# Kernel tuning notes

Measured on AMD Instinct MI355X. Metric: run time of the kernel, lower is better.

The kernel has to match this reference:

```python
import jax, jax.numpy as jnp
import numpy as np

N = 100000
E = 1600000
D = 128
L = 4
G = 64
EPS = 1e-5


def _bn(x, g, b, m, v):
    # BatchNorm1d in eval mode: normalize with running stats
    return (x - m) * jax.lax.rsqrt(v + EPS) * g + b


def setup_inputs() -> dict:
    key = jax.random.key(0)
    ks = jax.random.split(key, 32)
    x = jax.random.normal(ks[0], (N, 11), jnp.float32)
    pos = jax.random.normal(ks[1], (N, 3), jnp.float32)
    edge_index = jax.random.randint(ks[2], (2, E), 0, N)
    edge_attr = jax.random.normal(ks[3], (E, 4), jnp.float32)
    batch = jnp.sort(jax.random.randint(ks[4], (N,), 0, G))
    s = 0.05
    lin_in_w = jax.random.normal(ks[5], (14, D), jnp.float32) * s
    lin_in_b = jnp.zeros((D,), jnp.float32)
    msg_w1 = jax.random.normal(ks[6], (L, 2 * D + 4, D), jnp.float32) * s
    msg_b1 = jnp.zeros((L, D), jnp.float32)
    msg_bn_g = jnp.ones((L, D), jnp.float32)
    msg_bn_b = jnp.zeros((L, D), jnp.float32)
    msg_bn_m = jax.random.normal(ks[7], (L, D), jnp.float32) * s
    msg_bn_v = jax.random.uniform(ks[8], (L, D), jnp.float32, 0.5, 1.5)
    msg_w2 = jax.random.normal(ks[9], (L, D, D), jnp.float32) * s
    msg_b2 = jnp.zeros((L, D), jnp.float32)
    upd_w1 = jax.random.normal(ks[10], (L, 2 * D, D), jnp.float32) * s
    upd_b1 = jnp.zeros((L, D), jnp.float32)
    upd_bn_g = jnp.ones((L, D), jnp.float32)
    upd_bn_b = jnp.zeros((L, D), jnp.float32)
    upd_bn_m = jax.random.normal(ks[11], (L, D), jnp.float32) * s
    upd_bn_v = jax.random.uniform(ks[12], (L, D), jnp.float32, 0.5, 1.5)
    upd_w2 = jax.random.normal(ks[13], (L, D, D), jnp.float32) * s
    upd_b2 = jnp.zeros((L, D), jnp.float32)
    pred_w = jax.random.normal(ks[14], (D, 1), jnp.float32) * s
    pred_b = jnp.zeros((1,), jnp.float32)
    return dict(x=x, pos=pos, edge_index=edge_index, edge_attr=edge_attr, batch=batch,
                lin_in_w=lin_in_w, lin_in_b=lin_in_b,
                msg_w1=msg_w1, msg_b1=msg_b1, msg_bn_g=msg_bn_g, msg_bn_b=msg_bn_b,
                msg_bn_m=msg_bn_m, msg_bn_v=msg_bn_v, msg_w2=msg_w2, msg_b2=msg_b2,
                upd_w1=upd_w1, upd_b1=upd_b1, upd_bn_g=upd_bn_g, upd_bn_b=upd_bn_b,
                upd_bn_m=upd_bn_m, upd_bn_v=upd_bn_v, upd_w2=upd_w2, upd_b2=upd_b2,
                pred_w=pred_w, pred_b=pred_b)


def reference(x, pos, edge_index, edge_attr, batch,
              lin_in_w, lin_in_b,
              msg_w1, msg_b1, msg_bn_g, msg_bn_b, msg_bn_m, msg_bn_v, msg_w2, msg_b2,
              upd_w1, upd_b1, upd_bn_g, upd_bn_b, upd_bn_m, upd_bn_v, upd_w2, upd_b2,
              pred_w, pred_b):
    src = edge_index[0]  # j (source)
    dst = edge_index[1]  # i (target, aggregation index)
    h = jnp.concatenate([x, pos], axis=-1) @ lin_in_w + lin_in_b  # [N, D]
    for l in range(L):
        # message: cat(h_i, h_j, edge_attr) -> Linear -> ReLU -> BN -> Linear -> ReLU
        m = jnp.concatenate([h[dst], h[src], edge_attr], axis=-1)  # [E, 2D+4]
        m = jax.nn.relu(m @ msg_w1[l] + msg_b1[l])
        m = _bn(m, msg_bn_g[l], msg_bn_b[l], msg_bn_m[l], msg_bn_v[l])
        m = jax.nn.relu(m @ msg_w2[l] + msg_b2[l])  # [E, D]
        # aggregate: scatter-add on target nodes
        aggr = jax.ops.segment_sum(m, dst, num_segments=N)  # [N, D]
        # update: cat(h, aggr) -> Linear -> ReLU -> BN -> Linear -> ReLU
        u = jnp.concatenate([h, aggr], axis=-1)
        u = jax.nn.relu(u @ upd_w1[l] + upd_b1[l])
        u = _bn(u, upd_bn_g[l], upd_bn_b[l], upd_bn_m[l], upd_bn_v[l])
        u = jax.nn.relu(u @ upd_w2[l] + upd_b2[l])
        h = h + u  # residual
    # global mean pool over graphs
    sums = jax.ops.segment_sum(h, batch, num_segments=G)
    cnts = jax.ops.segment_sum(jnp.ones((N,), h.dtype), batch, num_segments=G)
    h_graph = sums / jnp.maximum(cnts, 1.0)[:, None]
    out = h_graph @ pred_w + pred_b  # [G, 1]
    return out.reshape(-1)
```

## Files before the change

### kernel.cpp

```cpp
#include <hip/hip_runtime.h>
#include <hip/hip_bf16.h>


#define EPSBN 1e-5f
#define TS 136
#define AS 264

typedef __bf16 bf16x8 __attribute__((ext_vector_type(8)));
typedef float floatx4 __attribute__((ext_vector_type(4)));

static __device__ __forceinline__ unsigned short f2b(float f) {
  union { float f; unsigned u; } v; v.f = f;
  unsigned u = v.u;
  return (unsigned short)((u + 0x7fffu + ((u >> 16) & 1u)) >> 16);
}
static __device__ __forceinline__ unsigned pk2(float lo, float hi) {
  union { __hip_bfloat162 h; unsigned u; } v;
  v.h = __float22bfloat162_rn(make_float2(lo, hi));
  return v.u;
}
static __device__ __forceinline__ float ubits(unsigned u) {
  union { unsigned u; float f; } v; v.u = u; return v.f;
}

__global__ __launch_bounds__(128) void fold_kernel(
    const float* __restrict__ mw2, const float* __restrict__ mb2,
    const float* __restrict__ mg, const float* __restrict__ mb,
    const float* __restrict__ mm, const float* __restrict__ mv,
    const float* __restrict__ uw2, const float* __restrict__ ub2,
    const float* __restrict__ ug, const float* __restrict__ ub,
    const float* __restrict__ um, const float* __restrict__ uv,
    unsigned short* __restrict__ mW2fT, float* __restrict__ mB2f,
    unsigned short* __restrict__ uW2fT, float* __restrict__ uB2f) {
  int l = blockIdx.x & 3;
  bool isu = blockIdx.x >= 4;
  const float* W2 = (isu ? uw2 : mw2) + (size_t)l * 128 * 128;
  const float* b2 = (isu ? ub2 : mb2) + l * 128;
  const float* gg = (isu ? ug : mg) + l * 128;
  const float* bb = (isu ? ub : mb) + l * 128;
  const float* mn = (isu ? um : mm) + l * 128;
  const float* vr = (isu ? uv : mv) + l * 128;
  unsigned short* WfT = (isu ? uW2fT : mW2fT) + (size_t)l * 128 * 128;
  float* Bf = (isu ? uB2f : mB2f) + l * 128;
  __shared__ float a[128], c[128];
  int d = threadIdx.x;
  float ad = gg[d] * rsqrtf(vr[d] + EPSBN);
  a[d] = ad;
  c[d] = bb[d] - mn[d] * ad;
  __syncthreads();
  float acc = b2[d];
  for (int k = 0; k < 128; ++k) {
    float w = W2[k * 128 + d];
    WfT[(size_t)d * 128 + k] = f2b(a[k] * w);
    acc = fmaf(c[k], w, acc);
  }
  Bf[d] = acc;
}

__global__ __launch_bounds__(256) void transp_kernel(
    const float* __restrict__ mw1, const float* __restrict__ uw1,
    unsigned short* __restrict__ W1abT, unsigned short* __restrict__ U1T) {
  int l = blockIdx.x & 3;
  bool isu = blockIdx.x >= 4;
  int tid = threadIdx.x;
  if (!isu) {
    const float* W = mw1 + (size_t)l * 260 * 128;
    unsigned short* T = W1abT + (size_t)l * 256 * 128;
    for (int i = tid; i < 256 * 128; i += 256) {
      int n = i >> 7, k = i & 127;
      float v = (n < 128) ? W[(size_t)k * 128 + n] : W[(size_t)(128 + k) * 128 + (n - 128)];
      T[i] = f2b(v);
    }
  } else {
    const float* W = uw1 + (size_t)l * 256 * 128;
    unsigned short* T = U1T + (size_t)l * 128 * 256;
    for (int i = tid; i < 128 * 256; i += 256) {
      int n = i >> 8, k = i & 255;
      T[i] = f2b(W[(size_t)k * 128 + n]);
    }
  }
}

__global__ __launch_bounds__(256) void lin_in_kernel(
    const float* __restrict__ x, const float* __restrict__ pos,
    const float* __restrict__ W, const float* __restrict__ b,
    float* __restrict__ h, int Nn) {
  int gi = blockIdx.x * 256 + threadIdx.x;
  if (gi >= Nn * 128) return;
  int n = gi >> 7, d = gi & 127;
  float acc = b[d];
#pragma unroll
  for (int j = 0; j < 11; ++j) acc = fmaf(x[(size_t)n * 11 + j], W[j * 128 + d], acc);
#pragma unroll
  for (int j = 0; j < 3; ++j) acc = fmaf(pos[(size_t)n * 3 + j], W[(11 + j) * 128 + d], acc);
  h[gi] = acc;
}

__global__ __launch_bounds__(256) void hist_kernel(const int* __restrict__ dst, int* __restrict__ count, int Ee) {
  int i = blockIdx.x * 256 + threadIdx.x;
  if (i < Ee) atomicAdd(&count[dst[i]], 1);
}

__global__ __launch_bounds__(1024) void scan1_kernel(
    const int* __restrict__ count, int* __restrict__ cursor, int* __restrict__ bsum, int n) {
  __shared__ int buf[1024];
  int i = blockIdx.x * 1024 + threadIdx.x;
  int v = (i < n) ? count[i] : 0;
  buf[threadIdx.x] = v;
  __syncthreads();
  for (int off = 1; off < 1024; off <<= 1) {
    int t = (threadIdx.x >= off) ? buf[threadIdx.x - off] : 0;
    __syncthreads();
    buf[threadIdx.x] += t;
    __syncthreads();
  }
  if (i < n) cursor[i] = buf[threadIdx.x] - v;
  if (threadIdx.x == 1023) bsum[blockIdx.x] = buf[1023];
}
__global__ __launch_bounds__(1024) void scan2_kernel(int* __restrict__ bsum, int nb) {
  __shared__ int buf[1024];
  int v = (threadIdx.x < nb) ? bsum[threadIdx.x] : 0;
  buf[threadIdx.x] = v;
  __syncthreads();
  for (int off = 1; off < 1024; off <<= 1) {
    int t = (threadIdx.x >= off) ? buf[threadIdx.x - off] : 0;
    __syncthreads();
    buf[threadIdx.x] += t;
    __syncthreads();
  }
  if (threadIdx.x < nb) bsum[threadIdx.x] = buf[threadIdx.x] - v;
}
__global__ __launch_bounds__(1024) void scan3_kernel(
    int* __restrict__ cursor, const int* __restrict__ bsum, int n) {
  int i = blockIdx.x * 1024 + threadIdx.x;
  if (i < n) cursor[i] += bsum[blockIdx.x];
}

__global__ __launch_bounds__(256) void scatter_kernel(
    const int* __restrict__ src, const int* __restrict__ dst, const float* __restrict__ ea,
    int* __restrict__ cursor, int* __restrict__ dst_s, int* __restrict__ src_s,
    float* __restrict__ ea_s, int Ee) {
  int e = blockIdx.x * 256 + threadIdx.x;
  if (e >= Ee) return;
  int dn = dst[e];
  int pos = atomicAdd(&cursor[dn], 1);
  dst_s[pos] = dn;
  src_s[pos] = src[e];
  *(float4*)(ea_s + (size_t)pos * 4) = *(const float4*)(ea + (size_t)e * 4);
}

__global__ __launch_bounds__(256) void mask_kernel(
    const int* __restrict__ dst_s, unsigned long long* __restrict__ masks, int Ee, int nt) {
  int tile = blockIdx.x * 4 + (threadIdx.x >> 6);
  int lane = threadIdx.x & 63;
  if (tile >= nt) return;
  int e = tile * 64 + lane;
  bool start;
  if (e >= Ee || lane == 0) start = true;
  else start = (dst_s[e] != dst_s[e - 1]);
  unsigned long long m = __ballot(start);
  if (lane == 0) masks[tile] = m;
}

__global__ __launch_bounds__(256) void pq_kernel(
    const float* __restrict__ h, const unsigned short* __restrict__ W1abT,
    unsigned short* __restrict__ P, unsigned short* __restrict__ Q, int Nn) {
  __shared__ unsigned short hs[64 * TS];
  const int tid = threadIdx.x;
  const int row0 = blockIdx.x * 64;
#pragma unroll
  for (int i = 0; i < 8; ++i) {
    int idx = tid + i * 256;
    int r = idx >> 5, c4 = (idx & 31) << 2;
    float4 v = make_float4(0.f, 0.f, 0.f, 0.f);
    if (row0 + r < Nn) v = *(const float4*)(h + (size_t)(row0 + r) * 128 + c4);
    *(uint2*)&hs[r * TS + c4] = make_uint2(pk2(v.x, v.y), pk2(v.z, v.w));
  }
  __syncthreads();
  const int lane = tid & 63, wv = tid >> 6;
  const int m16 = lane & 15, quad = lane >> 4;
  floatx4 acc[4][4];
#pragma unroll
  for (int mt = 0; mt < 4; ++mt)
#pragma unroll
    for (int nt = 0; nt < 4; ++nt) acc[mt][nt] = (floatx4)(0.0f);
  const __bf16* WT = (const __bf16*)W1abT;
  const __bf16* TlB = (const __bf16*)hs;
#pragma unroll
  for (int kb = 0; kb < 4; ++kb) {
    bf16x8 a[4], w[4];
#pragma unroll
    for (int mt = 0; mt < 4; ++mt)
      a[mt] = *(const bf16x8*)(TlB + (16 * mt + m16) * TS + kb * 32 + quad * 8);
#pragma unroll
    for (int nt = 0; nt < 4; ++nt)
      w[nt] = *(const bf16x8*)(WT + (size_t)(64 * wv + 16 * nt + m16) * 128 + kb * 32 + quad * 8);
#pragma unroll
    for (int mt = 0; mt < 4; ++mt)
#pragma unroll
      for (int nt = 0; nt < 4; ++nt)
        acc[mt][nt] = __builtin_amdgcn_mfma_f32_16x16x32_bf16(w[nt], a[mt], acc[mt][nt], 0, 0, 0);
  }
#pragma unroll
  for (int mt = 0; mt < 4; ++mt) {
    int row = row0 + 16 * mt + m16;
    if (row >= Nn) continue;
#pragma unroll
    for (int nt = 0; nt < 4; ++nt) {
      int n0 = 64 * wv + 16 * nt + 4 * quad;
      floatx4 A = acc[mt][nt];
      uint2 o = make_uint2(pk2(A[0], A[1]), pk2(A[2], A[3]));
      if (n0 < 128) *(uint2*)(P + (size_t)row * 128 + n0) = o;
      else *(uint2*)(Q + (size_t)row * 128 + (n0 - 128)) = o;
    }
  }
}

static __device__ __forceinline__ void gather_pq(
    const unsigned short* __restrict__ P, const unsigned short* __restrict__ Q,
    const int* __restrict__ sdstBase, const int* __restrict__ ssrcBase,
    int rw, int c0, uint4* pv, uint4* qv) {
#pragma unroll
  for (int p = 0; p < 4; ++p) {
    int slot = 16 * p + rw;
    int dn = sdstBase[slot];
    int dna = dn < 0 ? 0 : dn;
    int sna = ssrcBase[slot];
    pv[p] = *(const uint4*)(P + (size_t)dna * 128 + c0);
    qv[p] = *(const uint4*)(Q + (size_t)sna * 128 + c0);
  }
}

static __device__ __forceinline__ void build_T(
    unsigned short* __restrict__ TlBuf,
    const uint4* pv, const uint4* qv,
    const int* __restrict__ sdstBase, const float* __restrict__ seaBase,
    const float wc[4][8], const float b1r[8], int rw, int c0) {
#pragma unroll
  for (int p = 0; p < 4; ++p) {
    int row = 16 * p + rw;
    int dn = sdstBase[row];
    uint4 out = make_uint4(0u, 0u, 0u, 0u);
    if (dn >= 0) {
      float e0f = seaBase[row * 4 + 0], e1f = seaBase[row * 4 + 1];
      float e2f = seaBase[row * 4 + 2], e3f = seaBase[row * 4 + 3];
      unsigned pu[4] = {pv[p].x, pv[p].y, pv[p].z, pv[p].w};
      unsigned qu[4] = {qv[p].x, qv[p].y, qv[p].z, qv[p].w};
      unsigned ou[4];
#pragma unroll
      for (int g = 0; g < 4; ++g) {
        float plo = ubits(pu[g] << 16), phi = ubits(pu[g] & 0xffff0000u);
        float qlo = ubits(qu[g] << 16), qhi = ubits(qu[g] & 0xffff0000u);
        int j0 = 2 * g, j1 = 2 * g + 1;
        float t0 = plo + qlo + b1r[j0];
        float t1 = phi + qhi + b1r[j1];
        t0 = fmaf(e0f, wc[0][j0], fmaf(e1f, wc[1][j0], fmaf(e2f, wc[2][j0], fmaf(e3f, wc[3][j0], t0))));
        t1 = fmaf(e0f, wc[0][j1], fmaf(e1f, wc[1][j1], fmaf(e2f, wc[2][j1], fmaf(e3f, wc[3][j1], t1))));
        ou[g] = pk2(fmaxf(t0, 0.f), fmaxf(t1, 0.f));
      }
      out = make_uint4(ou[0], ou[1], ou[2], ou[3]);
    }
    *(uint4*)&TlBuf[row * TS + c0] = out;
  }
}

static __device__ __forceinline__ void mfma_B(
    const unsigned short* __restrict__ TlBuf, const __bf16* __restrict__ WT,
    int m16, int quad, int wv, floatx4 acc[4][2]) {
#pragma unroll
  for (int mt = 0; mt < 4; ++mt) { acc[mt][0] = (floatx4)(0.0f); acc[mt][1] = (floatx4)(0.0f); }
  const __bf16* TlB = (const __bf16*)TlBuf;
#pragma unroll
  for (int kb = 0; kb < 4; ++kb) {
    bf16x8 w0 = *(const bf16x8*)(WT + (size_t)(32 * wv + m16) * 128 + kb * 32 + quad * 8);
    bf16x8 w1 = *(const bf16x8*)(WT + (size_t)(32 * wv + 16 + m16) * 128 + kb * 32 + quad * 8);
    bf16x8 a[4];
#pragma unroll
    for (int mt = 0; mt < 4; ++mt)
      a[mt] = *(const bf16x8*)(TlB + (16 * mt + m16) * TS + kb * 32 + quad * 8);
#pragma unroll
    for (int mt = 0; mt < 4; ++mt) {
      acc[mt][0] = __builtin_amdgcn_mfma_f32_16x16x32_bf16(w0, a[mt], acc[mt][0], 0, 0, 0);
      acc[mt][1] = __builtin_amdgcn_mfma_f32_16x16x32_bf16(w1, a[mt], acc[mt][1], 0, 0, 0);
    }
  }
}

static __device__ __forceinline__ void epi_m(
    unsigned short* __restrict__ TlBuf, floatx4 acc[4][2],
    const float* __restrict__ B2f, int m16, int quad, int wv) {
  int n0 = 32 * wv + 4 * quad;
  float4 bv0 = *(const float4*)(B2f + n0);
  float4 bv1 = *(const float4*)(B2f + n0 + 16);
#pragma unroll
  for (int mt = 0; mt < 4; ++mt) {
    int row = 16 * mt + m16;
    floatx4 A0 = acc[mt][0], A1 = acc[mt][1];
    *(uint2*)&TlBuf[row * TS + n0] =
        make_uint2(pk2(fmaxf(A0[0] + bv0.x, 0.f), fmaxf(A0[1] + bv0.y, 0.f)),
                   pk2(fmaxf(A0[2] + bv0.z, 0.f), fmaxf(A0[3] + bv0.w, 0.f)));
    *(uint2*)&TlBuf[row * TS + n0 + 16] =
        make_uint2(pk2(fmaxf(A1[0] + bv1.x, 0.f), fmaxf(A1[1] + bv1.y, 0.f)),
                   pk2(fmaxf(A1[2] + bv1.z, 0.f), fmaxf(A1[3] + bv1.w, 0.f)));
  }
}

static __device__ __forceinline__ void seg_reduce(
    const unsigned short* __restrict__ TlBuf, const int* __restrict__ sdstBase,
    unsigned long long mask, float* __restrict__ aggr, int tid) {
  const int c4 = (tid & 15) << 2;
  const int st = tid >> 4;
  const int dfirst = sdstBase[0], dlast = sdstBase[63];
  for (int s = st; s < 64; s += 16) {
    if (!(mask & (1ull << s))) continue;
    int dn = sdstBase[s];
    if (dn < 0) continue;
    int end;
    if (s >= 63) end = 64;
    else {
      unsigned long long m2 = mask >> (s + 1);
      end = m2 ? (s + 1 + (int)__builtin_ctzll(m2)) : 64;
    }
    float a0 = 0.f, a1 = 0.f, a2 = 0.f, a3 = 0.f, a4 = 0.f, a5 = 0.f, a6 = 0.f, a7 = 0.f;
    for (int e = s; e < end; ++e) {
      uint2 v1 = *(const uint2*)&TlBuf[e * TS + c4];
      uint2 v2 = *(const uint2*)&TlBuf[e * TS + 64 + c4];
      a0 += ubits(v1.x << 16); a1 += ubits(v1.x & 0xffff0000u);
      a2 += ubits(v1.y << 16); a3 += ubits(v1.y & 0xffff0000u);
      a4 += ubits(v2.x << 16); a5 += ubits(v2.x & 0xffff0000u);
      a6 += ubits(v2.y << 16); a7 += ubits(v2.y & 0xffff0000u);
    }
    float* ap = aggr + (size_t)dn * 128 + c4;
    if (dn == dfirst || dn == dlast) {
      atomicAdd(ap + 0, a0); atomicAdd(ap + 1, a1);
      atomicAdd(ap + 2, a2); atomicAdd(ap + 3, a3);
      atomicAdd(ap + 64, a4); atomicAdd(ap + 65, a5);
      atomicAdd(ap + 66, a6); atomicAdd(ap + 67, a7);
    } else {
      *(float4*)ap = make_float4(a0, a1, a2, a3);
      *(float4*)(ap + 64) = make_float4(a4, a5, a6, a7);
    }
  }
}

__global__ __launch_bounds__(256, 3) void edge_kernel(
    const unsigned short* __restrict__ P, const unsigned short* __restrict__ Q,
    const float* __restrict__ ea_s, const int* __restrict__ dst_s, const int* __restrict__ src_s,
    const unsigned long long* __restrict__ masks,
    const float* __restrict__ W1c, const float* __restrict__ b1,
    const unsigned short* __restrict__ W2fT, const float* __restrict__ B2f,
    float* __restrict__ aggr, int Ee, int nT) {
  __shared__ unsigned short Tl[2][64 * TS];
  __shared__ float sea[128 * 4];
  __shared__ int sdst[128], ssrc[128];
  const int tid = threadIdx.x;
  int b = blockIdx.x;
  const int nB = gridDim.x;
  const int per = nB >> 3;
  if (b < (per << 3)) b = (b & 7) * per + (b >> 3);
  const int t0 = b * 2, t1 = t0 + 1;
  const int e0 = t0 * 64;
  const bool has1 = (t1 < nT);
  const unsigned long long mask0 = masks[t0];
  const unsigned long long mask1 = has1 ? masks[t1] : 0ull;
  if (tid < 128) {
    int e = e0 + tid;
    bool ok = e < Ee;
    sdst[tid] = ok ? dst_s[e] : -1;
    ssrc[tid] = ok ? src_s[e] : 0;
    float4 ev = ok ? *(const float4*)(ea_s + (size_t)e * 4) : make_float4(0.f, 0.f, 0.f, 0.f);
    *(float4*)&sea[tid * 4] = ev;
  }
  const int rw = tid >> 4, c0 = (tid & 15) << 3;
  float wc[4][8], b1r[8];
#pragma unroll
  for (int r = 0; r < 4; ++r) {
    *(float4*)&wc[r][0] = *(const float4*)(W1c + r * 128 + c0);
    *(float4*)&wc[r][4] = *(const float4*)(W1c + r * 128 + c0 + 4);
  }
  *(float4*)&b1r[0] = *(const float4*)(b1 + c0);
  *(float4*)&b1r[4] = *(const float4*)(b1 + c0 + 4);
  __syncthreads();

  const int lane = tid & 63, wv = tid >> 6;
  const int m16 = lane & 15, quad = lane >> 4;
  const __bf16* WT = (const __bf16*)W2fT;

  uint4 pv[4], qv[4], pv1[4], qv1[4];
  gather_pq(P, Q, sdst, ssrc, rw, c0, pv, qv);
  build_T(Tl[0], pv, qv, sdst, sea, wc, b1r, rw, c0);
  if (has1) gather_pq(P, Q, sdst + 64, ssrc + 64, rw, c0, pv1, qv1);
  __syncthreads();

  floatx4 acc[4][2];
  mfma_B(Tl[0], WT, m16, quad, wv, acc);
  if (has1) build_T(Tl[1], pv1, qv1, sdst + 64, sea + 256, wc, b1r, rw, c0);
  __syncthreads();

  epi_m(Tl[0], acc, B2f, m16, quad, wv);
  floatx4 acc1[4][2];
  if (has1) mfma_B(Tl[1], WT, m16, quad, wv, acc1);
  __syncthreads();

  seg_reduce(Tl[0], sdst, mask0, aggr, tid);
  if (has1) {
    epi_m(Tl[1], acc1, B2f, m16, quad, wv);
    __syncthreads();
    seg_reduce(Tl[1], sdst + 64, mask1, aggr, tid);
  }
}

__global__ __launch_bounds__(256) void upd_kernel(
    float* __restrict__ h, const float* __restrict__ aggr,
    const unsigned short* __restrict__ U1T, const float* __restrict__ ub1,
    const unsigned short* __restrict__ uW2fT, const float* __restrict__ uB2f, int Nn,
    const unsigned short* __restrict__ W1abT_next,
    unsigned short* __restrict__ P, unsigned short* __restrict__ Q) {
  __shared__ unsigned short as_[64 * AS];
  const int tid = threadIdx.x;
  const int row0 = blockIdx.x * 64;
#pragma unroll
  for (int i = 0; i < 8; ++i) {
    int idx = tid + i * 256;
    int r = idx >> 5, c4 = (idx & 31) << 2;
    float4 v = make_float4(0.f, 0.f, 0.f, 0.f);
    if (row0 + r < Nn) v = *(const float4*)(h + (size_t)(row0 + r) * 128 + c4);
    *(uint2*)&as_[r * AS + c4] = make_uint2(pk2(v.x, v.y), pk2(v.z, v.w));
  }
#pragma unroll
  for (int i = 0; i < 8; ++i) {
    int idx = tid + i * 256;
    int r = idx >> 5, c4 = (idx & 31) << 2;
    float4 v = make_float4(0.f, 0.f, 0.f, 0.f);
    if (row0 + r < Nn) v = *(const float4*)(aggr + (size_t)(row0 + r) * 128 + c4);
    *(uint2*)&as_[r * AS + 128 + c4] = make_uint2(pk2(v.x, v.y), pk2(v.z, v.w));
  }
  __syncthreads();
  const int lane = tid & 63, wv = tid >> 6;
  const int m16 = lane & 15, quad = lane >> 4;
  const __bf16* asB = (const __bf16*)as_;
  unsigned short* u1s = as_;
  {
    floatx4 acc[4][2];
#pragma unroll
    for (int mt = 0; mt < 4; ++mt) { acc[mt][0] = (floatx4)(0.0f); acc[mt][1] = (floatx4)(0.0f); }
    const __bf16* WT = (const __bf16*)U1T;
#pragma unroll
    for (int kb = 0; kb < 8; ++kb) {
      bf16x8 w0 = *(const bf16x8*)(WT + (size_t)(32 * wv + m16) * 256 + kb * 32 + quad * 8);
      bf16x8 w1 = *(const bf16x8*)(WT + (size_t)(32 * wv + 16 + m16) * 256 + kb * 32 + quad * 8);
      bf16x8 a[4];
#pragma unroll
      for (int mt = 0; mt < 4; ++mt)
        a[mt] = *(const bf16x8*)(asB + (16 * mt + m16) * AS + kb * 32 + quad * 8);
#pragma unroll
      for (int mt = 0; mt < 4; ++mt) {
        acc[mt][0] = __builtin_amdgcn_mfma_f32_16x16x32_bf16(w0, a[mt], acc[mt][0], 0, 0, 0);
        acc[mt][1] = __builtin_amdgcn_mfma_f32_16x16x32_bf16(w1, a[mt], acc[mt][1], 0, 0, 0);
      }
    }
    __syncthreads();
    int n0 = 32 * wv + 4 * quad;
    float4 bv0 = *(const float4*)(ub1 + n0);
    float4 bv1 = *(const float4*)(ub1 + n0 + 16);
#pragma unroll
    for (int mt = 0; mt < 4; ++mt) {
      int row = 16 * mt + m16;
      floatx4 A0 = acc[mt][0], A1 = acc[mt][1];
      *(uint2*)&u1s[row * TS + n0] =
          make_uint2(pk2(fmaxf(A0[0] + bv0.x, 0.f), fmaxf(A0[1] + bv0.y, 0.f)),
                     pk2(fmaxf(A0[2] + bv0.z, 0.f), fmaxf(A0[3] + bv0.w, 0.f)));
      *(uint2*)&u1s[row * TS + n0 + 16] =
          make_uint2(pk2(fmaxf(A1[0] + bv1.x, 0.f), fmaxf(A1[1] + bv1.y, 0.f)),
                     pk2(fmaxf(A1[2] + bv1.z, 0.f), fmaxf(A1[3] + bv1.w, 0.f)));
    }
  }
  __syncthreads();
  {
    floatx4 acc[4][2];
#pragma unroll
    for (int mt = 0; mt < 4; ++mt) { acc[mt][0] = (floatx4)(0.0f); acc[mt][1] = (floatx4)(0.0f); }
    const __bf16* WT = (const __bf16*)uW2fT;
    const __bf16* u1B = (const __bf16*)u1s;
#pragma unroll
    for (int kb = 0; kb < 4; ++kb) {
      bf16x8 w0 = *(const bf16x8*)(WT + (size_t)(32 * wv + m16) * 128 + kb * 32 + quad * 8);
      bf16x8 w1 = *(const bf16x8*)(WT + (size_t)(32 * wv + 16 + m16) * 128 + kb * 32 + quad * 8);
      bf16x8 a[4];
#pragma unroll
      for (int mt = 0; mt < 4; ++mt)
        a[mt] = *(const bf16x8*)(u1B + (16 * mt + m16) * TS + kb * 32 + quad * 8);
#pragma unroll
      for (int mt = 0; mt < 4; ++mt) {
        acc[mt][0] = __builtin_amdgcn_mfma_f32_16x16x32_bf16(w0, a[mt], acc[mt][0], 0, 0, 0);
        acc[mt][1] = __builtin_amdgcn_mfma_f32_16x16x32_bf16(w1, a[mt], acc[mt][1], 0, 0, 0);
      }
    }
    __syncthreads();
    int n0 = 32 * wv + 4 * quad;
    float4 bv0 = *(const float4*)(uB2f + n0);
    float4 bv1 = *(const float4*)(uB2f + n0 + 16);
#pragma unroll
    for (int mt = 0; mt < 4; ++mt) {
      int rloc = 16 * mt + m16;
      int row = row0 + rloc;
      floatx4 A0 = acc[mt][0], A1 = acc[mt][1];
      if (row < Nn) {
        float* hp0 = h + (size_t)row * 128 + n0;
        float4 hv0 = *(float4*)hp0;
        float4 o0 = make_float4(hv0.x + fmaxf(A0[0] + bv0.x, 0.f), hv0.y + fmaxf(A0[1] + bv0.y, 0.f),
                                hv0.z + fmaxf(A0[2] + bv0.z, 0.f), hv0.w + fmaxf(A0[3] + bv0.w, 0.f));
        *(float4*)hp0 = o0;
        float* hp1 = hp0 + 16;
        float4 hv1 = *(float4*)hp1;
        float4 o1 = make_float4(hv1.x + fmaxf(A1[0] + bv1.x, 0.f), hv1.y + fmaxf(A1[1] + bv1.y, 0.f),
                                hv1.z + fmaxf(A1[2] + bv1.z, 0.f), hv1.w + fmaxf(A1[3] + bv1.w, 0.f));
        *(float4*)hp1 = o1;
        if (W1abT_next) {
          *(uint2*)&u1s[rloc * TS + n0] = make_uint2(pk2(o0.x, o0.y), pk2(o0.z, o0.w));
          *(uint2*)&u1s[rloc * TS + n0 + 16] = make_uint2(pk2(o1.x, o1.y), pk2(o1.z, o1.w));
        }
      } else if (W1abT_next) {
        *(uint2*)&u1s[rloc * TS + n0] = make_uint2(0u, 0u);
        *(uint2*)&u1s[rloc * TS + n0 + 16] = make_uint2(0u, 0u);
      }
    }
  }
  if (W1abT_next) {
    __syncthreads();
    floatx4 pacc[4][4];
#pragma unroll
    for (int mt = 0; mt < 4; ++mt)
#pragma unroll
      for (int nt = 0; nt < 4; ++nt) pacc[mt][nt] = (floatx4)(0.0f);
    const __bf16* WT = (const __bf16*)W1abT_next;
    const __bf16* hB = (const __bf16*)u1s;
#pragma unroll
    for (int kb = 0; kb < 4; ++kb) {
      bf16x8 a[4], w[4];
#pragma unroll
      for (int mt = 0; mt < 4; ++mt)
        a[mt] = *(const bf16x8*)(hB + (16 * mt + m16) * TS + kb * 32 + quad * 8);
#pragma unroll
      for (int nt = 0; nt < 4; ++nt)
        w[nt] = *(const bf16x8*)(WT + (size_t)(64 * wv + 16 * nt + m16) * 128 + kb * 32 + quad * 8);
#pragma unroll
      for (int mt = 0; mt < 4; ++mt)
#pragma unroll
        for (int nt = 0; nt < 4; ++nt)
          pacc[mt][nt] = __builtin_amdgcn_mfma_f32_16x16x32_bf16(w[nt], a[mt], pacc[mt][nt], 0, 0, 0);
    }
#pragma unroll
    for (int mt = 0; mt < 4; ++mt) {
      int row = row0 + 16 * mt + m16;
      if (row >= Nn) continue;
#pragma unroll
      for (int nt = 0; nt < 4; ++nt) {
        int n0 = 64 * wv + 16 * nt + 4 * quad;
        floatx4 A = pacc[mt][nt];
        uint2 o = make_uint2(pk2(A[0], A[1]), pk2(A[2], A[3]));
        if (n0 < 128) *(uint2*)(P + (size_t)row * 128 + n0) = o;
        else *(uint2*)(Q + (size_t)row * 128 + (n0 - 128)) = o;
      }
    }
  }
}

__global__ __launch_bounds__(128) void pool_sum_kernel(
    const float* __restrict__ h, const int* __restrict__ batch,
    float* __restrict__ sums, int* __restrict__ gcnt, int Nn) {
  int n0 = blockIdx.x * 256;
  if (n0 >= Nn) return;
  int nend = min(n0 + 256, Nn);
  int d = threadIdx.x;
  int gcur = batch[n0];
  float run = 0.f;
  int cnt = 0;
  for (int n = n0; n < nend; ++n) {
    int g = batch[n];
    if (g != gcur) {
      atomicAdd(&sums[(size_t)gcur * 128 + d], run);
      if (d == 0) atomicAdd(&gcnt[gcur], cnt);
      run = 0.f; cnt = 0; gcur = g;
    }
    run += h[(size_t)n * 128 + d];
    cnt += 1;
  }
  atomicAdd(&sums[(size_t)gcur * 128 + d], run);
  if (d == 0) atomicAdd(&gcnt[gcur], cnt);
}

__global__ __launch_bounds__(128) void pred_kernel(
    const float* __restrict__ sums, const int* __restrict__ gcnt,
    const float* __restrict__ pw, const float* __restrict__ pb, float* __restrict__ out) {
  __shared__ float red[2];
  int g = blockIdx.x, d = threadIdx.x;
  float c = fmaxf((float)gcnt[g], 1.f);
  float v = (sums[(size_t)g * 128 + d] / c) * pw[d];
  for (int o = 32; o > 0; o >>= 1) v += __shfl_down(v, o, 64);
  if ((d & 63) == 0) red[d >> 6] = v;
  __syncthreads();
  if (d == 0) out[g] = red[0] + red[1] + pb[0];
}

extern "C" void kernel_launch(void* const* d_in, const int* in_sizes, int n_in,
                              void* d_out, int out_size, void* d_ws, size_t ws_size,
                              hipStream_t stream) {
  const float* x = (const float*)d_in[0];
  const float* pos = (const float*)d_in[1];
  const int* ei = (const int*)d_in[2];
  const float* ea = (const float*)d_in[3];
  const int* batch = (const int*)d_in[4];
  const float* lin_w = (const float*)d_in[5];
  const float* lin_b = (const float*)d_in[6];
  const float* mw1 = (const float*)d_in[7];
  const float* mb1 = (const float*)d_in[8];
  const float* mg = (const float*)d_in[9];
  const float* mbb = (const float*)d_in[10];
  const float* mm = (const float*)d_in[11];
  const float* mv = (const float*)d_in[12];
  const float* mw2 = (const float*)d_in[13];
  const float* mb2 = (const float*)d_in[14];
  const float* uw1 = (const float*)d_in[15];
  const float* ub1 = (const float*)d_in[16];
  const float* ug = (const float*)d_in[17];
  const float* ubb = (const float*)d_in[18];
  const float* um = (const float*)d_in[19];
  const float* uv = (const float*)d_in[20];
  const float* uw2 = (const float*)d_in[21];
  const float* ub2 = (const float*)d_in[22];
  const float* pw = (const float*)d_in[23];
  const float* pb = (const float*)d_in[24];
  float* out = (float*)d_out;

  const int Nn = in_sizes[0] / 11;
  const int Ee = in_sizes[3] / 4;
  const int* srcp = ei;
  const int* dstp = ei + Ee;

  char* wsb = (char*)d_ws;
  size_t off = 0;
  auto alloc = [&](size_t bytes) -> void* {
    void* p = wsb + off;
    off = (off + bytes + 255) & ~(size_t)255;
    return p;
  };
  float* h = (float*)alloc((size_t)Nn * 128 * 4);
  unsigned short* Pb = (unsigned short*)alloc((size_t)Nn * 128 * 2);
  unsigned short* Qb = (unsigned short*)alloc((size_t)Nn * 128 * 2);
  float* aggr = (float*)alloc((size_t)Nn * 128 * 4);
  int* dst_s = (int*)alloc((size_t)Ee * 4);
  int* src_s = (int*)alloc((size_t)Ee * 4);
  float* ea_s = (float*)alloc((size_t)Ee * 16);
  int* count = (int*)alloc((size_t)Nn * 4);
  int* cursor = (int*)alloc((size_t)Nn * 4);
  int* bsum = (int*)alloc((size_t)1024 * 4);
  const int nTiles = (Ee + 63) / 64;
  unsigned long long* masks = (unsigned long long*)alloc((size_t)nTiles * 8);
  unsigned short* mW2fT = (unsigned short*)alloc((size_t)4 * 128 * 128 * 2);
  unsigned short* uW2fT = (unsigned short*)alloc((size_t)4 * 128 * 128 * 2);
  unsigned short* W1abT = (unsigned short*)alloc((size_t)4 * 256 * 128 * 2);
  unsigned short* U1T = (unsigned short*)alloc((size_t)4 * 128 * 256 * 2);
  float* mB2f = (float*)alloc((size_t)4 * 128 * 4);
  float* uB2f = (float*)alloc((size_t)4 * 128 * 4);
  float* sums = (float*)alloc((size_t)out_size * 128 * 4);
  int* gcnt = (int*)alloc((size_t)out_size * 4);
  (void)ws_size; (void)n_in;

  fold_kernel<<<8, 128, 0, stream>>>(mw2, mb2, mg, mbb, mm, mv,
                                     uw2, ub2, ug, ubb, um, uv,
                                     mW2fT, mB2f, uW2fT, uB2f);
  transp_kernel<<<8, 256, 0, stream>>>(mw1, uw1, W1abT, U1T);
  lin_in_kernel<<<(Nn * 128 + 255) / 256, 256, 0, stream>>>(x, pos, lin_w, lin_b, h, Nn);

  hipMemsetAsync(count, 0, (size_t)Nn * 4, stream);
  hist_kernel<<<(Ee + 255) / 256, 256, 0, stream>>>(dstp, count, Ee);
  const int NB = (Nn + 1023) / 1024;
  scan1_kernel<<<NB, 1024, 0, stream>>>(count, cursor, bsum, Nn);
  scan2_kernel<<<1, 1024, 0, stream>>>(bsum, NB);
  scan3_kernel<<<NB, 1024, 0, stream>>>(cursor, bsum, Nn);
  scatter_kernel<<<(Ee + 255) / 256, 256, 0, stream>>>(srcp, dstp, ea, cursor,
                                                       dst_s, src_s, ea_s, Ee);
  mask_kernel<<<(nTiles + 3) / 4, 256, 0, stream>>>(dst_s, masks, Ee, nTiles);

  const int gN = (Nn + 63) / 64;
  pq_kernel<<<gN, 256, 0, stream>>>(h, W1abT, Pb, Qb, Nn);
  for (int l = 0; l < 4; ++l) {
    hipMemsetAsync(aggr, 0, (size_t)Nn * 128 * 4, stream);
    edge_kernel<<<(nTiles + 1) / 2, 256, 0, stream>>>(
        Pb, Qb, ea_s, dst_s, src_s, masks,
        mw1 + (size_t)l * 260 * 128 + 256 * 128, mb1 + l * 128,
        mW2fT + (size_t)l * 16384, mB2f + l * 128, aggr, Ee, nTiles);
    upd_kernel<<<gN, 256, 0, stream>>>(
        h, aggr, U1T + (size_t)l * 128 * 256, ub1 + l * 128,
        uW2fT + (size_t)l * 16384, uB2f + l * 128, Nn,
        (l < 3) ? (W1abT + (size_t)(l + 1) * 256 * 128) : nullptr, Pb, Qb);
  }

  hipMemsetAsync(sums, 0, (size_t)out_size * 128 * 4, stream);
  hipMemsetAsync(gcnt, 0, (size_t)out_size * 4, stream);
  pool_sum_kernel<<<(Nn + 255) / 256, 128, 0, stream>>>(h, batch, sums, gcnt, Nn);
  pred_kernel<<<out_size, 128, 0, stream>>>(sums, gcnt, pw, pb, out);
}
```

Before: 1.933 ms.

## Make edge kernel persistent with per-XCD work counters and cross-pair prefetch

Turns the edge kernel into a persistent grid of 1024 blocks. Blocks pull tile pairs from per-XCD atomic counters, and the next pair's edge metadata and P/Q gathers are prefetched while the current pair's MFMA and segment reduction run. The W2 MFMA fragments and the biases are now loaded into registers once per block instead of once per tile. The elementwise edge-build, epilogue and segment-reduce code switches to packed float2 math, with the segment reduce using wider 16-byte LDS reads. This trades higher register pressure, which may cut occupancy, and an extra atomic and memset per layer for less launch, tail and gather-latency cost.

```diff
diff --git a/kernel.cpp b/kernel.cpp
--- a/kernel.cpp
+++ b/kernel.cpp
@@ -8,6 +8,20 @@
 
 typedef __bf16 bf16x8 __attribute__((ext_vector_type(8)));
 typedef float floatx4 __attribute__((ext_vector_type(4)));
+typedef float f32x2 __attribute__((ext_vector_type(2)));
+
+#if __has_builtin(__builtin_elementwise_fma)
+#define VFMA(a, b, c) __builtin_elementwise_fma((a), (b), (c))
+#else
+#define VFMA(a, b, c) ((a) * (b) + (c))
+#endif
+#if __has_builtin(__builtin_elementwise_max)
+#define VMAX(a, b) __builtin_elementwise_max((a), (b))
+#else
+static __device__ __forceinline__ f32x2 VMAX(f32x2 a, f32x2 b) {
+  f32x2 r; r.x = fmaxf(a.x, b.x); r.y = fmaxf(a.y, b.y); return r;
+}
+#endif
 
 static __device__ __forceinline__ unsigned short f2b(float f) {
   union { float f; unsigned u; } v; v.f = f;
@@ -21,6 +35,13 @@
 }
 static __device__ __forceinline__ float ubits(unsigned u) {
   union { unsigned u; float f; } v; v.u = u; return v.f;
+}
+static __device__ __forceinline__ f32x2 mk2(float a, float b) {
+  f32x2 r; r.x = a; r.y = b; return r;
+}
+static __device__ __forceinline__ f32x2 sp2(float a) { return mk2(a, a); }
+static __device__ __forceinline__ f32x2 up2(unsigned u) {
+  return mk2(ubits(u << 16), ubits(u & 0xffff0000u));
 }
 
 __global__ __launch_bounds__(128) void fold_kernel(
@@ -235,28 +256,27 @@
     unsigned short* __restrict__ TlBuf,
     const uint4* pv, const uint4* qv,
     const int* __restrict__ sdstBase, const float* __restrict__ seaBase,
-    const float wc[4][8], const float b1r[8], int rw, int c0) {
+    const f32x2 (*__restrict__ wc2)[4], const f32x2* __restrict__ b1v, int rw, int c0) {
 #pragma unroll
   for (int p = 0; p < 4; ++p) {
     int row = 16 * p + rw;
     int dn = sdstBase[row];
     uint4 out = make_uint4(0u, 0u, 0u, 0u);
     if (dn >= 0) {
-      float e0f = seaBase[row * 4 + 0], e1f = seaBase[row * 4 + 1];
-      float e2f = seaBase[row * 4 + 2], e3f = seaBase[row * 4 + 3];
+      float e0 = seaBase[row * 4 + 0], e1 = seaBase[row * 4 + 1];
+      float e2 = seaBase[row * 4 + 2], e3 = seaBase[row * 4 + 3];
       unsigned pu[4] = {pv[p].x, pv[p].y, pv[p].z, pv[p].w};
       unsigned qu[4] = {qv[p].x, qv[p].y, qv[p].z, qv[p].w};
       unsigned ou[4];
 #pragma unroll
       for (int g = 0; g < 4; ++g) {
-        float plo = ubits(pu[g] << 16), phi = ubits(pu[g] & 0xffff0000u);
-        float qlo = ubits(qu[g] << 16), qhi = ubits(qu[g] & 0xffff0000u);
-        int j0 = 2 * g, j1 = 2 * g + 1;
-        float t0 = plo + qlo + b1r[j0];
-        float t1 = phi + qhi + b1r[j1];
-        t0 = fmaf(e0f, wc[0][j0], fmaf(e1f, wc[1][j0], fmaf(e2f, wc[2][j0], fmaf(e3f, wc[3][j0], t0))));
-        t1 = fmaf(e0f, wc[0][j1], fmaf(e1f, wc[1][j1], fmaf(e2f, wc[2][j1], fmaf(e3f, wc[3][j1], t1))));
-        ou[g] = pk2(fmaxf(t0, 0.f), fmaxf(t1, 0.f));
+        f32x2 t = up2(pu[g]) + up2(qu[g]) + b1v[g];
+        t = VFMA(sp2(e0), wc2[0][g], t);
+        t = VFMA(sp2(e1), wc2[1][g], t);
+        t = VFMA(sp2(e2), wc2[2][g], t);
+        t = VFMA(sp2(e3), wc2[3][g], t);
+        t = VMAX(t, sp2(0.f));
+        ou[g] = pk2(t.x, t.y);
       }
       out = make_uint4(ou[0], ou[1], ou[2], ou[3]);
     }
@@ -265,50 +285,46 @@
 }
 
 static __device__ __forceinline__ void mfma_B(
-    const unsigned short* __restrict__ TlBuf, const __bf16* __restrict__ WT,
-    int m16, int quad, int wv, floatx4 acc[4][2]) {
+    const unsigned short* __restrict__ TlBuf, const bf16x8 (*__restrict__ wA)[2],
+    int m16, int quad, floatx4 acc[4][2]) {
 #pragma unroll
   for (int mt = 0; mt < 4; ++mt) { acc[mt][0] = (floatx4)(0.0f); acc[mt][1] = (floatx4)(0.0f); }
   const __bf16* TlB = (const __bf16*)TlBuf;
 #pragma unroll
   for (int kb = 0; kb < 4; ++kb) {
-    bf16x8 w0 = *(const bf16x8*)(WT + (size_t)(32 * wv + m16) * 128 + kb * 32 + quad * 8);
-    bf16x8 w1 = *(const bf16x8*)(WT + (size_t)(32 * wv + 16 + m16) * 128 + kb * 32 + quad * 8);
     bf16x8 a[4];
 #pragma unroll
     for (int mt = 0; mt < 4; ++mt)
       a[mt] = *(const bf16x8*)(TlB + (16 * mt + m16) * TS + kb * 32 + quad * 8);
 #pragma unroll
     for (int mt = 0; mt < 4; ++mt) {
-      acc[mt][0] = __builtin_amdgcn_mfma_f32_16x16x32_bf16(w0, a[mt], acc[mt][0], 0, 0, 0);
-      acc[mt][1] = __builtin_amdgcn_mfma_f32_16x16x32_bf16(w1, a[mt], acc[mt][1], 0, 0, 0);
+      acc[mt][0] = __builtin_amdgcn_mfma_f32_16x16x32_bf16(wA[kb][0], a[mt], acc[mt][0], 0, 0, 0);
+      acc[mt][1] = __builtin_amdgcn_mfma_f32_16x16x32_bf16(wA[kb][1], a[mt], acc[mt][1], 0, 0, 0);
     }
   }
 }
 
 static __device__ __forceinline__ void epi_m(
     unsigned short* __restrict__ TlBuf, floatx4 acc[4][2],
-    const float* __restrict__ B2f, int m16, int quad, int wv) {
+    const f32x2* __restrict__ bz, int m16, int quad, int wv) {
   int n0 = 32 * wv + 4 * quad;
-  float4 bv0 = *(const float4*)(B2f + n0);
-  float4 bv1 = *(const float4*)(B2f + n0 + 16);
 #pragma unroll
   for (int mt = 0; mt < 4; ++mt) {
     int row = 16 * mt + m16;
     floatx4 A0 = acc[mt][0], A1 = acc[mt][1];
-    *(uint2*)&TlBuf[row * TS + n0] =
-        make_uint2(pk2(fmaxf(A0[0] + bv0.x, 0.f), fmaxf(A0[1] + bv0.y, 0.f)),
-                   pk2(fmaxf(A0[2] + bv0.z, 0.f), fmaxf(A0[3] + bv0.w, 0.f)));
-    *(uint2*)&TlBuf[row * TS + n0 + 16] =
-        make_uint2(pk2(fmaxf(A1[0] + bv1.x, 0.f), fmaxf(A1[1] + bv1.y, 0.f)),
-                   pk2(fmaxf(A1[2] + bv1.z, 0.f), fmaxf(A1[3] + bv1.w, 0.f)));
+    f32x2 t0 = VMAX(mk2(A0[0], A0[1]) + bz[0], sp2(0.f));
+    f32x2 t1 = VMAX(mk2(A0[2], A0[3]) + bz[1], sp2(0.f));
+    f32x2 t2 = VMAX(mk2(A1[0], A1[1]) + bz[2], sp2(0.f));
+    f32x2 t3 = VMAX(mk2(A1[2], A1[3]) + bz[3], sp2(0.f));
+    *(uint2*)&TlBuf[row * TS + n0] = make_uint2(pk2(t0.x, t0.y), pk2(t1.x, t1.y));
+    *(uint2*)&TlBuf[row * TS + n0 + 16] = make_uint2(pk2(t2.x, t2.y), pk2(t3.x, t3.y));
   }
 }
 
 static __device__ __forceinline__ void seg_reduce(
     const unsigned short* __restrict__ TlBuf, const int* __restrict__ sdstBase,
     unsigned long long mask, float* __restrict__ aggr, int tid) {
-  const int c4 = (tid & 15) << 2;
+  const int c8 = (tid & 15) << 3;
   const int st = tid >> 4;
   const int dfirst = sdstBase[0], dlast = sdstBase[63];
   for (int s = st; s < 64; s += 16) {
@@ -321,25 +337,39 @@
       unsigned long long m2 = mask >> (s + 1);
       end = m2 ? (s + 1 + (int)__builtin_ctzll(m2)) : 64;
     }
-    float a0 = 0.f, a1 = 0.f, a2 = 0.f, a3 = 0.f, a4 = 0.f, a5 = 0.f, a6 = 0.f, a7 = 0.f;
+    f32x2 a0 = sp2(0.f), a1 = sp2(0.f), a2 = sp2(0.f), a3 = sp2(0.f);
     for (int e = s; e < end; ++e) {
-      uint2 v1 = *(const uint2*)&TlBuf[e * TS + c4];
-      uint2 v2 = *(const uint2*)&TlBuf[e * TS + 64 + c4];
-      a0 += ubits(v1.x << 16); a1 += ubits(v1.x & 0xffff0000u);
-      a2 += ubits(v1.y << 16); a3 += ubits(v1.y & 0xffff0000u);
-      a4 += ubits(v2.x << 16); a5 += ubits(v2.x & 0xffff0000u);
-      a6 += ubits(v2.y << 16); a7 += ubits(v2.y & 0xffff0000u);
-    }
-    float* ap = aggr + (size_t)dn * 128 + c4;
+      uint4 v = *(const uint4*)&TlBuf[e * TS + c8];
+      a0 += up2(v.x); a1 += up2(v.y); a2 += up2(v.z); a3 += up2(v.w);
+    }
+    float* ap = aggr + (size_t)dn * 128 + c8;
     if (dn == dfirst || dn == dlast) {
-      atomicAdd(ap + 0, a0); atomicAdd(ap + 1, a1);
-      atomicAdd(ap + 2, a2); atomicAdd(ap + 3, a3);
-      atomicAdd(ap + 64, a4); atomicAdd(ap + 65, a5);
-      atomicAdd(ap + 66, a6); atomicAdd(ap + 67, a7);
+      atomicAdd(ap + 0, a0.x); atomicAdd(ap + 1, a0.y);
+      atomicAdd(ap + 2, a1.x); atomicAdd(ap + 3, a1.y);
+      atomicAdd(ap + 4, a2.x); atomicAdd(ap + 5, a2.y);
+      atomicAdd(ap + 6, a3.x); atomicAdd(ap + 7, a3.y);
     } else {
-      *(float4*)ap = make_float4(a0, a1, a2, a3);
-      *(float4*)(ap + 64) = make_float4(a4, a5, a6, a7);
-    }
+      *(float4*)ap = make_float4(a0.x, a0.y, a1.x, a1.y);
+      *(float4*)(ap + 4) = make_float4(a2.x, a2.y, a3.x, a3.y);
+    }
+  }
+}
+
+static __device__ __forceinline__ void stage_meta(
+    int pp, const int* __restrict__ dst_s, const int* __restrict__ src_s,
+    const float* __restrict__ ea_s, int Ee, int tid,
+    int* __restrict__ sdsth, int* __restrict__ ssrc, float* __restrict__ sea) {
+  if (tid < 128) {
+    int e = pp * 128 + tid;
+    bool ok = e < Ee;
+    sdsth[tid] = ok ? dst_s[e] : -1;
+    ssrc[tid] = ok ? src_s[e] : 0;
+  } else {
+    int t2 = tid - 128;
+    int e = pp * 128 + t2;
+    float4 ev = (e < Ee) ? *(const float4*)(ea_s + (size_t)e * 4)
+                         : make_float4(0.f, 0.f, 0.f, 0.f);
+    *(float4*)&sea[t2 * 4] = ev;
   }
 }
 
@@ -349,64 +379,95 @@
     const unsigned long long* __restrict__ masks,
     const float* __restrict__ W1c, const float* __restrict__ b1,
     const unsigned short* __restrict__ W2fT, const float* __restrict__ B2f,
-    float* __restrict__ aggr, int Ee, int nT) {
+    float* __restrict__ aggr, int Ee, int nT, int* __restrict__ ctr) {
   __shared__ unsigned short Tl[2][64 * TS];
   __shared__ float sea[128 * 4];
-  __shared__ int sdst[128], ssrc[128];
+  __shared__ int sdst[2][128], ssrc[128];
+  __shared__ int snext;
   const int tid = threadIdx.x;
-  int b = blockIdx.x;
-  const int nB = gridDim.x;
-  const int per = nB >> 3;
-  if (b < (per << 3)) b = (b & 7) * per + (b >> 3);
-  const int t0 = b * 2, t1 = t0 + 1;
-  const int e0 = t0 * 64;
-  const bool has1 = (t1 < nT);
-  const unsigned long long mask0 = masks[t0];
-  const unsigned long long mask1 = has1 ? masks[t1] : 0ull;
-  if (tid < 128) {
-    int e = e0 + tid;
-    bool ok = e < Ee;
-    sdst[tid] = ok ? dst_s[e] : -1;
-    ssrc[tid] = ok ? src_s[e] : 0;
-    float4 ev = ok ? *(const float4*)(ea_s + (size_t)e * 4) : make_float4(0.f, 0.f, 0.f, 0.f);
-    *(float4*)&sea[tid * 4] = ev;
-  }
-  const int rw = tid >> 4, c0 = (tid & 15) << 3;
-  float wc[4][8], b1r[8];
-#pragma unroll
-  for (int r = 0; r < 4; ++r) {
-    *(float4*)&wc[r][0] = *(const float4*)(W1c + r * 128 + c0);
-    *(float4*)&wc[r][4] = *(const float4*)(W1c + r * 128 + c0 + 4);
-  }
-  *(float4*)&b1r[0] = *(const float4*)(b1 + c0);
-  *(float4*)&b1r[4] = *(const float4*)(b1 + c0 + 4);
-  __syncthreads();
-
   const int lane = tid & 63, wv = tid >> 6;
   const int m16 = lane & 15, quad = lane >> 4;
+  const int rw = tid >> 4, c0 = (tid & 15) << 3;
+
+  const int nPairs = (nT + 1) >> 1;
+  const int xcd = blockIdx.x & 7;
+  const int perX = (nPairs + 7) >> 3;
+  const int lo = xcd * perX;
+  const int hi = min(lo + perX, nPairs);
+
+  if (tid == 0) snext = lo + atomicAdd(&ctr[xcd], 1);
+
+  f32x2 wc2[4][4], b1v[4];
+#pragma unroll
+  for (int r = 0; r < 4; ++r) {
+    float4 u = *(const float4*)(W1c + r * 128 + c0);
+    float4 v = *(const float4*)(W1c + r * 128 + c0 + 4);
+    wc2[r][0] = mk2(u.x, u.y); wc2[r][1] = mk2(u.z, u.w);
+    wc2[r][2] = mk2(v.x, v.y); wc2[r][3] = mk2(v.z, v.w);
+  }
+  {
+    float4 u = *(const float4*)(b1 + c0);
+    float4 v = *(const float4*)(b1 + c0 + 4);
+    b1v[0] = mk2(u.x, u.y); b1v[1] = mk2(u.z, u.w);
+    b1v[2] = mk2(v.x, v.y); b1v[3] = mk2(v.z, v.w);
+  }
   const __bf16* WT = (const __bf16*)W2fT;
+  bf16x8 wA[4][2];
+#pragma unroll
+  for (int kb = 0; kb < 4; ++kb) {
+    wA[kb][0] = *(const bf16x8*)(WT + (size_t)(32 * wv + m16) * 128 + kb * 32 + quad * 8);
+    wA[kb][1] = *(const bf16x8*)(WT + (size_t)(32 * wv + 16 + m16) * 128 + kb * 32 + quad * 8);
+  }
+  f32x2 bz[4];
+  {
+    int n0e = 32 * wv + 4 * quad;
+    float4 b0 = *(const float4*)(B2f + n0e);
+    float4 b1q = *(const float4*)(B2f + n0e + 16);
+    bz[0] = mk2(b0.x, b0.y); bz[1] = mk2(b0.z, b0.w);
+    bz[2] = mk2(b1q.x, b1q.y); bz[3] = mk2(b1q.z, b1q.w);
+  }
+
+  __syncthreads();
+  int cp = snext;
+  if (cp >= hi) return;
+  stage_meta(cp, dst_s, src_s, ea_s, Ee, tid, sdst[0], ssrc, sea);
+  __syncthreads();
 
   uint4 pv[4], qv[4], pv1[4], qv1[4];
-  gather_pq(P, Q, sdst, ssrc, rw, c0, pv, qv);
-  build_T(Tl[0], pv, qv, sdst, sea, wc, b1r, rw, c0);
-  if (has1) gather_pq(P, Q, sdst + 64, ssrc + 64, rw, c0, pv1, qv1);
-  __syncthreads();
-
-  floatx4 acc[4][2];
-  mfma_B(Tl[0], WT, m16, quad, wv, acc);
-  if (has1) build_T(Tl[1], pv1, qv1, sdst + 64, sea + 256, wc, b1r, rw, c0);
-  __syncthreads();
-
-  epi_m(Tl[0], acc, B2f, m16, quad, wv);
-  floatx4 acc1[4][2];
-  if (has1) mfma_B(Tl[1], WT, m16, quad, wv, acc1);
-  __syncthreads();
-
-  seg_reduce(Tl[0], sdst, mask0, aggr, tid);
-  if (has1) {
-    epi_m(Tl[1], acc1, B2f, m16, quad, wv);
-    __syncthreads();
-    seg_reduce(Tl[1], sdst + 64, mask1, aggr, tid);
+  gather_pq(P, Q, sdst[0], ssrc, rw, c0, pv, qv);
+  int h = 0;
+  for (;;) {
+    const int ta = cp * 2;
+    const unsigned long long maskA = masks[ta];
+    const unsigned long long maskB = (ta + 1 < nT) ? masks[ta + 1] : 0ull;
+
+    build_T(Tl[0], pv, qv, sdst[h], sea, wc2, b1v, rw, c0);
+    if (tid == 0) snext = lo + atomicAdd(&ctr[xcd], 1);
+    gather_pq(P, Q, sdst[h] + 64, ssrc + 64, rw, c0, pv1, qv1);
+    __syncthreads();
+    const int np = snext;
+
+    floatx4 acc[4][2];
+    mfma_B(Tl[0], wA, m16, quad, acc);
+    build_T(Tl[1], pv1, qv1, sdst[h] + 64, sea + 256, wc2, b1v, rw, c0);
+    __syncthreads();
+
+    epi_m(Tl[0], acc, bz, m16, quad, wv);
+    floatx4 acc1[4][2];
+    mfma_B(Tl[1], wA, m16, quad, acc1);
+    if (np < hi)
+      stage_meta(np, dst_s, src_s, ea_s, Ee, tid, sdst[h ^ 1], ssrc, sea);
+    __syncthreads();
+
+    epi_m(Tl[1], acc1, bz, m16, quad, wv);
+    if (np < hi)
+      gather_pq(P, Q, sdst[h ^ 1], ssrc, rw, c0, pv, qv);
+    seg_reduce(Tl[0], sdst[h], maskA, aggr, tid);
+    __syncthreads();
+
+    seg_reduce(Tl[1], sdst[h] + 64, maskB, aggr, tid);
+    if (np >= hi) break;
+    cp = np; h ^= 1;
   }
 }
 
@@ -665,6 +726,7 @@
   float* uB2f = (float*)alloc((size_t)4 * 128 * 4);
   float* sums = (float*)alloc((size_t)out_size * 128 * 4);
   int* gcnt = (int*)alloc((size_t)out_size * 4);
+  int* ectr = (int*)alloc(32);
   (void)ws_size; (void)n_in;
 
   fold_kernel<<<8, 128, 0, stream>>>(mw2, mb2, mg, mbb, mm, mv,
@@ -687,10 +749,11 @@
   pq_kernel<<<gN, 256, 0, stream>>>(h, W1abT, Pb, Qb, Nn);
   for (int l = 0; l < 4; ++l) {
     hipMemsetAsync(aggr, 0, (size_t)Nn * 128 * 4, stream);
-    edge_kernel<<<(nTiles + 1) / 2, 256, 0, stream>>>(
+    hipMemsetAsync(ectr, 0, 32, stream);
+    edge_kernel<<<1024, 256, 0, stream>>>(
         Pb, Qb, ea_s, dst_s, src_s, masks,
         mw1 + (size_t)l * 260 * 128 + 256 * 128, mb1 + l * 128,
-        mW2fT + (size_t)l * 16384, mB2f + l * 128, aggr, Ee, nTiles);
+        mW2fT + (size_t)l * 16384, mB2f + l * 128, aggr, Ee, nTiles, ectr);
     upd_kernel<<<gN, 256, 0, stream>>>(
         h, aggr, U1T + (size_t)l * 128 * 256, ub1 + l * 128,
         uW2fT + (size_t)l * 16384, uB2f + l * 128, Nn,
```

Result: slower. 2.459 ms (+27.2%).
